# Optimization experiments

Hardware: AMD Instinct MI355X
Metric: run time of the kernel (lower is better)

## Reference

```python
import jax, jax.numpy as jnp
import numpy as np

N_NODES = 30000
IN_DIM = 8
HIDDEN = 64
HEADS1 = 8
OUT_DIM = 8
NEG_SLOPE = 0.2


def _glorot(key, shape):
    fan_in, fan_out = shape[0], shape[-1]
    lim = jnp.sqrt(6.0 / (fan_in + fan_out))
    return jax.random.uniform(key, shape, jnp.float32, -lim, lim)


def setup_inputs() -> dict:
    key = jax.random.key(0)
    ks = jax.random.split(key, 12)
    x = jax.random.normal(ks[0], (N_NODES, IN_DIM), jnp.float32)
    edge_index = jax.random.randint(ks[1], (2, 300000), 0, N_NODES, jnp.int32)
    # layer 1: in=8, out=HIDDEN per head, 8 heads, concat
    W1l = _glorot(ks[2], (IN_DIM, HEADS1 * HIDDEN))
    W1r = _glorot(ks[3], (IN_DIM, HEADS1 * HIDDEN))
    a1 = _glorot(ks[4], (HEADS1, HIDDEN))
    b1 = jnp.zeros((HEADS1 * HIDDEN,), jnp.float32)
    # layer 2: in=HEADS1*HIDDEN, out=OUT_DIM, 1 head
    W2l = _glorot(ks[5], (HEADS1 * HIDDEN, OUT_DIM))
    W2r = _glorot(ks[6], (HEADS1 * HIDDEN, OUT_DIM))
    a2 = _glorot(ks[7], (1, OUT_DIM))
    b2 = jnp.zeros((OUT_DIM,), jnp.float32)
    return {"x": x, "edge_index": edge_index, "W1l": W1l, "W1r": W1r,
            "a1": a1, "b1": b1, "W2l": W2l, "W2r": W2r, "a2": a2, "b2": b2}


def gatv2_layer(x, src, dst, Wl, Wr, att, bias, heads, out_ch):
    n = x.shape[0]
    xl = (x @ Wl).reshape(n, heads, out_ch)   # messages (source side)
    xr = (x @ Wr).reshape(n, heads, out_ch)   # target side
    h = jax.nn.leaky_relu(xl[src] + xr[dst], NEG_SLOPE)   # [E,H,C]
    e = jnp.einsum('ehc,hc->eh', h, att)                  # [E,H]
    # segment softmax over incoming edges per destination node
    m = jax.ops.segment_max(e, dst, num_segments=n)
    p = jnp.exp(e - m[dst])
    denom = jax.ops.segment_sum(p, dst, num_segments=n)
    alpha = p / denom[dst]                                # [E,H]
    out = jax.ops.segment_sum(alpha[..., None] * xl[src], dst, num_segments=n)
    return out.reshape(n, heads * out_ch) + bias


def reference(x, edge_index, W1l, W1r, a1, b1, W2l, W2r, a2, b2):
    n = x.shape[0]
    loops = jnp.arange(n, dtype=edge_index.dtype)
    src = jnp.concatenate([edge_index[0], loops])  # add_self_loops=True (PyG default)
    dst = jnp.concatenate([edge_index[1], loops])
    h = gatv2_layer(x, src, dst, W1l, W1r, a1, b1, HEADS1, HIDDEN)
    h = jax.nn.relu(h)
    out = gatv2_layer(h, src, dst, W2l, W2r, a2, b2, 1, OUT_DIM)
    return out
```

## Files before the change

kernel.cpp:

```cpp
#include <hip/hip_runtime.h>
#include <hip/hip_fp16.h>
#include <math.h>

#define N_NODES   30000
#define N_EDGE    300000
#define N_EDGE_T  330000
#define HEADS     8
#define HIDDEN    64
#define IN_DIM    8
#define OUT_DIM   8
#define NEG_SLOPE 0.2f

#define DPP_ADDF(x, ctrl)                                                     \
    x += __int_as_float(__builtin_amdgcn_update_dpp(                          \
            0, __float_as_int(x), (ctrl), 0xF, 0xF, true))
#define RED16(x) do { DPP_ADDF(x, 0xB1); DPP_ADDF(x, 0x4E);                   \
                      DPP_ADDF(x, 0x141); DPP_ADDF(x, 0x140); } while (0)
#define RED8(x)  do { DPP_ADDF(x, 0xB1); DPP_ADDF(x, 0x4E);                   \
                      DPP_ADDF(x, 0x141); } while (0)


__global__ __launch_bounds__(256) void zero_kernel(int* __restrict__ count) {
    int i = blockIdx.x * 256 + threadIdx.x;
    if (i < N_NODES) count[i] = 0;
}

__global__ __launch_bounds__(256) void count_kernel(const int* __restrict__ ei,
                                                    int* __restrict__ count) {
    int e = blockIdx.x * 256 + threadIdx.x;
    if (e >= N_EDGE_T) return;
    int d = (e < N_EDGE) ? ei[N_EDGE + e] : (e - N_EDGE);
    atomicAdd(&count[d], 1);
}

__global__ __launch_bounds__(1024) void scan_kernel(const int* __restrict__ count,
                                                    int* __restrict__ row_start,
                                                    int* __restrict__ cursor) {
    __shared__ int wsum[16];
    const int tid  = threadIdx.x;
    const int wave = tid >> 6;
    const int lane = tid & 63;
    const int4* c4 = (const int4*)count;
    const int N4 = N_NODES / 4;
    int run = 0;
    for (int r = 0; r < 4; ++r) {
        const int g  = r * 1024 + tid;
        const int i0 = 2 * g;
        const int i1 = 2 * g + 1;
        int4 v0 = make_int4(0,0,0,0), v1 = make_int4(0,0,0,0);
        if (i0 < N4) v0 = c4[i0];
        if (i1 < N4) v1 = c4[i1];
        int s = v0.x + v0.y + v0.z + v0.w + v1.x + v1.y + v1.z + v1.w;
        int sc = s;
        #pragma unroll
        for (int off = 1; off < 64; off <<= 1) {
            int t = __shfl_up(sc, off, 64);
            if (lane >= off) sc += t;
        }
        if (lane == 63) wsum[wave] = sc;
        __syncthreads();
        if (tid < 16) {
            int w = wsum[tid];
            #pragma unroll
            for (int off = 1; off < 16; off <<= 1) {
                int t = __shfl_up(w, off, 64);
                if (tid >= off) w += t;
            }
            wsum[tid] = w;
        }
        __syncthreads();
        const int woff = (wave > 0) ? wsum[wave - 1] : 0;
        int e0 = run + woff + (sc - s);
        int4 ex0, ex1;
        ex0.x = e0;           ex0.y = ex0.x + v0.x;
        ex0.z = ex0.y + v0.y; ex0.w = ex0.z + v0.z;
        int e4 = ex0.w + v0.w;
        ex1.x = e4;           ex1.y = ex1.x + v1.x;
        ex1.z = ex1.y + v1.y; ex1.w = ex1.z + v1.z;
        if (i0 < N4) { ((int4*)row_start)[i0] = ex0; ((int4*)cursor)[i0] = ex0; }
        if (i1 < N4) { ((int4*)row_start)[i1] = ex1; ((int4*)cursor)[i1] = ex1; }
        const int tot = wsum[15];
        __syncthreads();
        run += tot;
    }
    if (tid == 0) row_start[N_NODES] = run;
}

__global__ __launch_bounds__(256) void scatter_kernel(const int* __restrict__ ei,
                                                      int* __restrict__ cursor,
                                                      int* __restrict__ edge_src) {
    int e = blockIdx.x * 256 + threadIdx.x;
    if (e >= N_EDGE_T) return;
    int s, d;
    if (e < N_EDGE) { s = ei[e]; d = ei[N_EDGE + e]; }
    else            { s = d = e - N_EDGE; }
    int pos = atomicAdd(&cursor[d], 1);
    edge_src[pos] = s;
}


__global__ __launch_bounds__(256) void proj_kernel(
    const float* __restrict__ x, const float* __restrict__ W1l,
    __half* __restrict__ xl_h)
{
    const int t    = threadIdx.x;
    const int lane = t & 63;
    float w0[IN_DIM], w1[IN_DIM];
    #pragma unroll
    for (int k = 0; k < IN_DIM; ++k) {
        const float2 wp = *(const float2*)&W1l[k * 512 + 2 * t];
        w0[k] = wp.x; w1[k] = wp.y;
    }
    for (int n = blockIdx.x; n < N_NODES; n += gridDim.x) {
        const float xlane = x[n * IN_DIM + (lane & 7)];
        float l0 = 0.f, l1 = 0.f;
        #pragma unroll
        for (int k = 0; k < IN_DIM; ++k) {
            const float xk = __shfl(xlane, k, 64);
            l0 = fmaf(xk, w0[k], l0);
            l1 = fmaf(xk, w1[k], l1);
        }
        ((__half2*)xl_h)[n * 256 + t] = __floats2half2_rn(l0, l1);
    }
}


__global__ void __launch_bounds__(256, 4)
layer1_kernel(
    const float* __restrict__ x,
    const __half* __restrict__ xl_h, const float* __restrict__ W1r,
    const float* __restrict__ a1,  const float* __restrict__ b1,
    const float* __restrict__ W2l, const float* __restrict__ W2r,
    const int* __restrict__ row_start, const int* __restrict__ edge_src,
    float* __restrict__ xl2, float* __restrict__ xr2)
{
    const int wv   = threadIdx.x >> 6;
    const int lane = threadIdx.x & 63;
    const int d    = blockIdx.x * 4 + wv;
    const int colb = lane * 8;

    const int rse = row_start[d + (lane & 1)];
    const int rs  = __shfl(rse, 0, 64);
    const int re  = __shfl(rse, 1, 64);
    const int deg = re - rs;
    const int nb  = deg < 64 ? deg : 64;

    const int eidx = edge_src[rs + (lane < deg ? lane : deg - 1)];

    const float xlane = x[d * IN_DIM + (lane & 7)];

    float av[8], xr[8];
    { const float4 a0 = *(const float4*)&a1[colb];
      const float4 a4 = *(const float4*)&a1[colb + 4];
      av[0]=a0.x; av[1]=a0.y; av[2]=a0.z; av[3]=a0.w;
      av[4]=a4.x; av[5]=a4.y; av[6]=a4.z; av[7]=a4.w; }
    #pragma unroll
    for (int i = 0; i < 8; ++i) xr[i] = 0.f;
    #pragma unroll
    for (int k = 0; k < IN_DIM; ++k) {
        const float xv = __shfl(xlane, k, 64);
        const float4 r0 = *(const float4*)&W1r[k * 512 + colb];
        const float4 r4 = *(const float4*)&W1r[k * 512 + colb + 4];
        xr[0] = fmaf(xv, r0.x, xr[0]); xr[1] = fmaf(xv, r0.y, xr[1]);
        xr[2] = fmaf(xv, r0.z, xr[2]); xr[3] = fmaf(xv, r0.w, xr[3]);
        xr[4] = fmaf(xv, r4.x, xr[4]); xr[5] = fmaf(xv, r4.y, xr[5]);
        xr[6] = fmaf(xv, r4.z, xr[6]); xr[7] = fmaf(xv, r4.w, xr[7]);
    }

    float denom  = 0.f;
    float acc[8] = {0.f,0.f,0.f,0.f,0.f,0.f,0.f,0.f};

    auto ldraw = [&](int j) -> int4 {
        const int s = __shfl(eidx, j, 64);
        return *(const int4*)(xl_h + (size_t)s * 512 + colb);
    };
    auto edge1 = [&](const int4 r, bool valid) {
        union { int i; __half2 h; } u0, u1, u2, u3;
        u0.i = r.x; u1.i = r.y; u2.i = r.z; u3.i = r.w;
        float rr[8]; float2 f;
        f = __half22float2(u0.h); rr[0] = f.x; rr[1] = f.y;
        f = __half22float2(u1.h); rr[2] = f.x; rr[3] = f.y;
        f = __half22float2(u2.h); rr[4] = f.x; rr[5] = f.y;
        f = __half22float2(u3.h); rr[6] = f.x; rr[7] = f.y;
        float e = 0.f;
        #pragma unroll
        for (int i = 0; i < 8; ++i) {
            const float q = rr[i] + xr[i];
            const float t = fmaxf(q, NEG_SLOPE * q);
            e = fmaf(av[i], t, e);
        }
        RED8(e);
        const float p = valid ? __expf(e) : 0.f;
        denom += p;
        #pragma unroll
        for (int i = 0; i < 8; ++i) acc[i] = fmaf(p, rr[i], acc[i]);
    };

    int4 R0, R1, R2, R3;
    {
        const int m = nb - 1;
        R0 = ldraw(0);
        R1 = ldraw(1 < m ? 1 : m);
        R2 = ldraw(2 < m ? 2 : m);
        R3 = ldraw(3 < m ? 3 : m);
    }
    for (int j = 0;; j += 4) {
        const bool more = j + 4 < nb;
        int4 N0, N1, N2, N3;
        if (more) {
            const int m = nb - 1;
            const int j4 = j + 4;
            N0 = ldraw(j4 < m ? j4 : m);
            N1 = ldraw(j4 + 1 < m ? j4 + 1 : m);
            N2 = ldraw(j4 + 2 < m ? j4 + 2 : m);
            N3 = ldraw(j4 + 3 < m ? j4 + 3 : m);
            __builtin_amdgcn_sched_barrier(0);
        }
        edge1(R0, true);
        edge1(R1, j + 1 < nb);
        edge1(R2, j + 2 < nb);
        edge1(R3, j + 3 < nb);
        if (!more) break;
        R0 = N0; R1 = N1; R2 = N2; R3 = N3;
    }
    for (int j = 64; j < deg; ++j) {
        const int s = edge_src[rs + j];
        const int4 r = *(const int4*)(xl_h + (size_t)s * 512 + colb);
        edge1(r, true);
    }

    const float inv = 1.f / denom;
    float hv[8];
    { const float4 b0 = *(const float4*)&b1[colb];
      const float4 b4 = *(const float4*)&b1[colb + 4];
      hv[0] = fmaxf(fmaf(acc[0], inv, b0.x), 0.f);
      hv[1] = fmaxf(fmaf(acc[1], inv, b0.y), 0.f);
      hv[2] = fmaxf(fmaf(acc[2], inv, b0.z), 0.f);
      hv[3] = fmaxf(fmaf(acc[3], inv, b0.w), 0.f);
      hv[4] = fmaxf(fmaf(acc[4], inv, b4.x), 0.f);
      hv[5] = fmaxf(fmaf(acc[5], inv, b4.y), 0.f);
      hv[6] = fmaxf(fmaf(acc[6], inv, b4.z), 0.f);
      hv[7] = fmaxf(fmaf(acc[7], inv, b4.w), 0.f); }

    float vl[OUT_DIM], vr[OUT_DIM];
    #pragma unroll
    for (int j = 0; j < OUT_DIM; ++j) { vl[j] = 0.f; vr[j] = 0.f; }
    #pragma unroll
    for (int i = 0; i < 8; ++i) {
        const int c = colb + i;
        const float4 l0 = *(const float4*)&W2l[c * OUT_DIM];
        const float4 l1 = *(const float4*)&W2l[c * OUT_DIM + 4];
        const float4 r0 = *(const float4*)&W2r[c * OUT_DIM];
        const float4 r1 = *(const float4*)&W2r[c * OUT_DIM + 4];
        const float h = hv[i];
        vl[0] = fmaf(h, l0.x, vl[0]); vl[1] = fmaf(h, l0.y, vl[1]);
        vl[2] = fmaf(h, l0.z, vl[2]); vl[3] = fmaf(h, l0.w, vl[3]);
        vl[4] = fmaf(h, l1.x, vl[4]); vl[5] = fmaf(h, l1.y, vl[5]);
        vl[6] = fmaf(h, l1.z, vl[6]); vl[7] = fmaf(h, l1.w, vl[7]);
        vr[0] = fmaf(h, r0.x, vr[0]); vr[1] = fmaf(h, r0.y, vr[1]);
        vr[2] = fmaf(h, r0.z, vr[2]); vr[3] = fmaf(h, r0.w, vr[3]);
        vr[4] = fmaf(h, r1.x, vr[4]); vr[5] = fmaf(h, r1.y, vr[5]);
        vr[6] = fmaf(h, r1.z, vr[6]); vr[7] = fmaf(h, r1.w, vr[7]);
    }
    #pragma unroll
    for (int j = 0; j < OUT_DIM; ++j) {
        RED16(vl[j]);
        vl[j] += __shfl_xor(vl[j], 16, 64);
        vl[j] += __shfl_xor(vl[j], 32, 64);
        RED16(vr[j]);
        vr[j] += __shfl_xor(vr[j], 16, 64);
        vr[j] += __shfl_xor(vr[j], 32, 64);
    }
    if (lane == 0) {
        *(float4*)&xl2[d * OUT_DIM]     = make_float4(vl[0], vl[1], vl[2], vl[3]);
        *(float4*)&xl2[d * OUT_DIM + 4] = make_float4(vl[4], vl[5], vl[6], vl[7]);
        *(float4*)&xr2[d * OUT_DIM]     = make_float4(vr[0], vr[1], vr[2], vr[3]);
        *(float4*)&xr2[d * OUT_DIM + 4] = make_float4(vr[4], vr[5], vr[6], vr[7]);
    }
}


__global__ __launch_bounds__(256) void layer2_kernel(
    const float* __restrict__ xl2, const float* __restrict__ xr2,
    const float* __restrict__ a2,  const float* __restrict__ b2,
    const int* __restrict__ row_start, const int* __restrict__ edge_src,
    float* __restrict__ out)
{
    const int wave = threadIdx.x >> 6;
    const int lane = threadIdx.x & 63;
    const int d = blockIdx.x * 4 + wave;
    if (d >= N_NODES) return;
    const int sub = lane >> 3;
    const int c   = lane & 7;

    const int rse = row_start[d + (lane & 1)];
    const int rs  = __shfl(rse, 0, 64);
    const int re  = __shfl(rse, 1, 64);

    const float a_c  = a2[c];
    const float xr_d = xr2[d * OUT_DIM + c];

    int  e0 = rs + sub;      const bool v0 = e0 < re; e0 = v0 ? e0 : re - 1;
    int  e1 = rs + 8 + sub;  const bool v1 = e1 < re; e1 = v1 ? e1 : re - 1;
    const int s0 = edge_src[e0];
    const int s1 = edge_src[e1];
    const float x0 = xl2[s0 * OUT_DIM + c];
    const float x1 = xl2[s1 * OUT_DIM + c];

    const float u0 = x0 + xr_d; const float t0 = fmaxf(u0, NEG_SLOPE * u0);
    const float u1 = x1 + xr_d; const float t1 = fmaxf(u1, NEG_SLOPE * u1);
    float g0 = a_c * t0;
    float g1 = a_c * t1;
    RED8(g0); RED8(g1);
    const float p0 = v0 ? __expf(g0) : 0.f;
    const float p1 = v1 ? __expf(g1) : 0.f;
    float denom = p0 + p1;
    float acc   = fmaf(p1, x1, p0 * x0);

    for (int b = rs + 16; b < re; b += 8) {
        int e = b + sub;
        const bool v = e < re; e = v ? e : re - 1;
        const int s = edge_src[e];
        const float xs = xl2[s * OUT_DIM + c];
        const float u = xs + xr_d;
        const float t = fmaxf(u, NEG_SLOPE * u);
        float g = a_c * t;
        RED8(g);
        const float p = v ? __expf(g) : 0.f;
        denom += p;
        acc = fmaf(p, xs, acc);
    }

    denom += __shfl_xor(denom, 8,  64);  acc += __shfl_xor(acc, 8,  64);
    denom += __shfl_xor(denom, 16, 64);  acc += __shfl_xor(acc, 16, 64);
    denom += __shfl_xor(denom, 32, 64);  acc += __shfl_xor(acc, 32, 64);

    if (sub == 0) out[d * OUT_DIM + c] = acc / denom + b2[c];
}


extern "C" void kernel_launch(void* const* d_in, const int* in_sizes, int n_in,
                              void* d_out, int out_size, void* d_ws, size_t ws_size,
                              hipStream_t stream) {
    const float* x   = (const float*)d_in[0];
    const int*   ei  = (const int*)  d_in[1];
    const float* W1l = (const float*)d_in[2];
    const float* W1r = (const float*)d_in[3];
    const float* a1  = (const float*)d_in[4];
    const float* b1  = (const float*)d_in[5];
    const float* W2l = (const float*)d_in[6];
    const float* W2r = (const float*)d_in[7];
    const float* a2  = (const float*)d_in[8];
    const float* b2  = (const float*)d_in[9];
    float* out = (float*)d_out;

    char* ws = (char*)d_ws;
    size_t off = 0;
    auto carve = [&](size_t bytes) { char* p = ws + off; off += (bytes + 255) & ~size_t(255); return p; };
    int*    count     = (int*)   carve(N_NODES * sizeof(int));
    int*    row_start = (int*)   carve((N_NODES + 1) * sizeof(int));
    int*    cursor    = (int*)   carve(N_NODES * sizeof(int));
    int*    edge_src  = (int*)   carve(N_EDGE_T * sizeof(int));
    float*  xl2       = (float*) carve(N_NODES * OUT_DIM * sizeof(float));
    float*  xr2       = (float*) carve(N_NODES * OUT_DIM * sizeof(float));
    __half* xl_h      = (__half*)carve((size_t)N_NODES * 512 * sizeof(__half));

    proj_kernel   <<<1024, 256, 0, stream>>>(x, W1l, xl_h);
    zero_kernel   <<<(N_NODES  + 255) / 256, 256, 0, stream>>>(count);
    count_kernel  <<<(N_EDGE_T + 255) / 256, 256, 0, stream>>>(ei, count);
    scan_kernel   <<<1, 1024, 0, stream>>>(count, row_start, cursor);
    scatter_kernel<<<(N_EDGE_T + 255) / 256, 256, 0, stream>>>(ei, cursor, edge_src);
    layer1_kernel <<<N_NODES / 4, 256, 0, stream>>>(x, xl_h, W1r, a1, b1, W2l, W2r,
                                                    row_start, edge_src, xl2, xr2);
    layer2_kernel <<<(N_NODES + 3) / 4, 256, 0, stream>>>(xl2, xr2, a2, b2,
                                                          row_start, edge_src, out);
}
```

Baseline: 292.6 us.

## Recompute source projections per edge instead of gathering precomputed fp16 features

Removes the separate projection kernel and its 30000x512 fp16 buffer. Layer 1 now gathers only the 8-float raw input row for each source node and recomputes the W1l projection per edge from register-held weights, broadcasting x values with readlane. The xr term is folded into the projection accumulator and subtracted back out at the end, since the attention weights sum to one. This swaps a heavy per-edge gather of 512 halfs for 64 FMAs per lane per edge and needs many more pinned registers, which may reduce occupancy.

```diff
diff --git a/kernel.cpp b/kernel.cpp
--- a/kernel.cpp
+++ b/kernel.cpp
@@ -1,5 +1,4 @@
 #include <hip/hip_runtime.h>
-#include <hip/hip_fp16.h>
 #include <math.h>
 
 #define N_NODES   30000
@@ -11,6 +10,8 @@
 #define OUT_DIM   8
 #define NEG_SLOPE 0.2f
 
+#define PIN_V(v) asm volatile("" : "+v"(v))
+
 #define DPP_ADDF(x, ctrl)                                                     \
     x += __int_as_float(__builtin_amdgcn_update_dpp(                          \
             0, __float_as_int(x), (ctrl), 0xF, 0xF, true))
@@ -18,6 +19,8 @@
                       DPP_ADDF(x, 0x141); DPP_ADDF(x, 0x140); } while (0)
 #define RED8(x)  do { DPP_ADDF(x, 0xB1); DPP_ADDF(x, 0x4E);                   \
                       DPP_ADDF(x, 0x141); } while (0)
+
+#define BCAST(v, C) __int_as_float(__builtin_amdgcn_readlane(__float_as_int(v), C))
 
 
 __global__ __launch_bounds__(256) void zero_kernel(int* __restrict__ count) {
@@ -99,36 +102,10 @@
 }
 
 
-__global__ __launch_bounds__(256) void proj_kernel(
-    const float* __restrict__ x, const float* __restrict__ W1l,
-    __half* __restrict__ xl_h)
-{
-    const int t    = threadIdx.x;
-    const int lane = t & 63;
-    float w0[IN_DIM], w1[IN_DIM];
-    #pragma unroll
-    for (int k = 0; k < IN_DIM; ++k) {
-        const float2 wp = *(const float2*)&W1l[k * 512 + 2 * t];
-        w0[k] = wp.x; w1[k] = wp.y;
-    }
-    for (int n = blockIdx.x; n < N_NODES; n += gridDim.x) {
-        const float xlane = x[n * IN_DIM + (lane & 7)];
-        float l0 = 0.f, l1 = 0.f;
-        #pragma unroll
-        for (int k = 0; k < IN_DIM; ++k) {
-            const float xk = __shfl(xlane, k, 64);
-            l0 = fmaf(xk, w0[k], l0);
-            l1 = fmaf(xk, w1[k], l1);
-        }
-        ((__half2*)xl_h)[n * 256 + t] = __floats2half2_rn(l0, l1);
-    }
-}
-
-
 __global__ void __launch_bounds__(256, 4)
 layer1_kernel(
     const float* __restrict__ x,
-    const __half* __restrict__ xl_h, const float* __restrict__ W1r,
+    const float* __restrict__ W1l, const float* __restrict__ W1r,
     const float* __restrict__ a1,  const float* __restrict__ b1,
     const float* __restrict__ W2l, const float* __restrict__ W2r,
     const int* __restrict__ row_start, const int* __restrict__ edge_src,
@@ -147,18 +124,28 @@
 
     const int eidx = edge_src[rs + (lane < deg ? lane : deg - 1)];
 
-    const float xlane = x[d * IN_DIM + (lane & 7)];
-
-    float av[8], xr[8];
+    const float xd = x[d * IN_DIM + (lane & 7)];
+
+    float wl[IN_DIM][8];
+    #pragma unroll
+    for (int k = 0; k < IN_DIM; ++k) {
+        const float4 l0 = *(const float4*)&W1l[k * 512 + colb];
+        const float4 l4 = *(const float4*)&W1l[k * 512 + colb + 4];
+        wl[k][0] = l0.x; wl[k][1] = l0.y; wl[k][2] = l0.z; wl[k][3] = l0.w;
+        wl[k][4] = l4.x; wl[k][5] = l4.y; wl[k][6] = l4.z; wl[k][7] = l4.w;
+    }
+    float av[8];
     { const float4 a0 = *(const float4*)&a1[colb];
       const float4 a4 = *(const float4*)&a1[colb + 4];
       av[0]=a0.x; av[1]=a0.y; av[2]=a0.z; av[3]=a0.w;
       av[4]=a4.x; av[5]=a4.y; av[6]=a4.z; av[7]=a4.w; }
+
+    float xr[8];
     #pragma unroll
     for (int i = 0; i < 8; ++i) xr[i] = 0.f;
     #pragma unroll
     for (int k = 0; k < IN_DIM; ++k) {
-        const float xv = __shfl(xlane, k, 64);
+        const float xv = BCAST(xd, k);
         const float4 r0 = *(const float4*)&W1r[k * 512 + colb];
         const float4 r4 = *(const float4*)&W1r[k * 512 + colb + 4];
         xr[0] = fmaf(xv, r0.x, xr[0]); xr[1] = fmaf(xv, r0.y, xr[1]);
@@ -167,80 +154,94 @@
         xr[6] = fmaf(xv, r4.z, xr[6]); xr[7] = fmaf(xv, r4.w, xr[7]);
     }
 
+    #pragma unroll
+    for (int k = 0; k < IN_DIM; ++k) {
+        #pragma unroll
+        for (int i = 0; i < 8; ++i) PIN_V(wl[k][i]);
+    }
+    #pragma unroll
+    for (int i = 0; i < 8; ++i) { PIN_V(av[i]); PIN_V(xr[i]); }
+
     float denom  = 0.f;
     float acc[8] = {0.f,0.f,0.f,0.f,0.f,0.f,0.f,0.f};
 
-    auto ldraw = [&](int j) -> int4 {
-        const int s = __shfl(eidx, j, 64);
-        return *(const int4*)(xl_h + (size_t)s * 512 + colb);
+    auto ldx = [&](int g) -> float {
+        const int sl = __shfl(eidx, (g << 3) + (lane >> 3), 64);
+        return x[(size_t)sl * IN_DIM + (lane & 7)];
     };
-    auto edge1 = [&](const int4 r, bool valid) {
-        union { int i; __half2 h; } u0, u1, u2, u3;
-        u0.i = r.x; u1.i = r.y; u2.i = r.z; u3.i = r.w;
-        float rr[8]; float2 f;
-        f = __half22float2(u0.h); rr[0] = f.x; rr[1] = f.y;
-        f = __half22float2(u1.h); rr[2] = f.x; rr[3] = f.y;
-        f = __half22float2(u2.h); rr[4] = f.x; rr[5] = f.y;
-        f = __half22float2(u3.h); rr[6] = f.x; rr[7] = f.y;
-        float e = 0.f;
-        #pragma unroll
-        for (int i = 0; i < 8; ++i) {
-            const float q = rr[i] + xr[i];
-            const float t = fmaxf(q, NEG_SLOPE * q);
-            e = fmaf(av[i], t, e);
-        }
+
+    auto edge_do = [&](float q0, float q1, float q2, float q3,
+                       float q4, float q5, float q6, float q7, bool valid) {
+        float t, e;
+        t = fmaxf(q0, NEG_SLOPE * q0); e = av[0] * t;
+        t = fmaxf(q1, NEG_SLOPE * q1); e = fmaf(av[1], t, e);
+        t = fmaxf(q2, NEG_SLOPE * q2); e = fmaf(av[2], t, e);
+        t = fmaxf(q3, NEG_SLOPE * q3); e = fmaf(av[3], t, e);
+        t = fmaxf(q4, NEG_SLOPE * q4); e = fmaf(av[4], t, e);
+        t = fmaxf(q5, NEG_SLOPE * q5); e = fmaf(av[5], t, e);
+        t = fmaxf(q6, NEG_SLOPE * q6); e = fmaf(av[6], t, e);
+        t = fmaxf(q7, NEG_SLOPE * q7); e = fmaf(av[7], t, e);
         RED8(e);
         const float p = valid ? __expf(e) : 0.f;
         denom += p;
+        acc[0] = fmaf(p, q0, acc[0]); acc[1] = fmaf(p, q1, acc[1]);
+        acc[2] = fmaf(p, q2, acc[2]); acc[3] = fmaf(p, q3, acc[3]);
+        acc[4] = fmaf(p, q4, acc[4]); acc[5] = fmaf(p, q5, acc[5]);
+        acc[6] = fmaf(p, q6, acc[6]); acc[7] = fmaf(p, q7, acc[7]);
+    };
+
+    float xg = ldx(0);
+    for (int g = 0;; ++g) {
+        const bool more = ((g + 1) << 3) < nb;
+        float xgn;
+        if (more) xgn = ldx(g + 1);
+
         #pragma unroll
-        for (int i = 0; i < 8; ++i) acc[i] = fmaf(p, rr[i], acc[i]);
-    };
-
-    int4 R0, R1, R2, R3;
-    {
-        const int m = nb - 1;
-        R0 = ldraw(0);
-        R1 = ldraw(1 < m ? 1 : m);
-        R2 = ldraw(2 < m ? 2 : m);
-        R3 = ldraw(3 < m ? 3 : m);
-    }
-    for (int j = 0;; j += 4) {
-        const bool more = j + 4 < nb;
-        int4 N0, N1, N2, N3;
-        if (more) {
-            const int m = nb - 1;
-            const int j4 = j + 4;
-            N0 = ldraw(j4 < m ? j4 : m);
-            N1 = ldraw(j4 + 1 < m ? j4 + 1 : m);
-            N2 = ldraw(j4 + 2 < m ? j4 + 2 : m);
-            N3 = ldraw(j4 + 3 < m ? j4 + 3 : m);
-            __builtin_amdgcn_sched_barrier(0);
+        for (int jj = 0; jj < 8; ++jj) {
+            const int j = (g << 3) + jj;
+            float q0 = xr[0], q1 = xr[1], q2 = xr[2], q3 = xr[3];
+            float q4 = xr[4], q5 = xr[5], q6 = xr[6], q7 = xr[7];
+            #pragma unroll
+            for (int k = 0; k < IN_DIM; ++k) {
+                const float xk = BCAST(xg, jj * 8 + k);
+                q0 = fmaf(xk, wl[k][0], q0); q1 = fmaf(xk, wl[k][1], q1);
+                q2 = fmaf(xk, wl[k][2], q2); q3 = fmaf(xk, wl[k][3], q3);
+                q4 = fmaf(xk, wl[k][4], q4); q5 = fmaf(xk, wl[k][5], q5);
+                q6 = fmaf(xk, wl[k][6], q6); q7 = fmaf(xk, wl[k][7], q7);
+            }
+            edge_do(q0, q1, q2, q3, q4, q5, q6, q7, j < nb);
         }
-        edge1(R0, true);
-        edge1(R1, j + 1 < nb);
-        edge1(R2, j + 2 < nb);
-        edge1(R3, j + 3 < nb);
         if (!more) break;
-        R0 = N0; R1 = N1; R2 = N2; R3 = N3;
+        xg = xgn;
     }
     for (int j = 64; j < deg; ++j) {
         const int s = edge_src[rs + j];
-        const int4 r = *(const int4*)(xl_h + (size_t)s * 512 + colb);
-        edge1(r, true);
+        const float xt = x[(size_t)s * IN_DIM + (lane & 7)];
+        float q0 = xr[0], q1 = xr[1], q2 = xr[2], q3 = xr[3];
+        float q4 = xr[4], q5 = xr[5], q6 = xr[6], q7 = xr[7];
+        #pragma unroll
+        for (int k = 0; k < IN_DIM; ++k) {
+            const float xk = BCAST(xt, k);
+            q0 = fmaf(xk, wl[k][0], q0); q1 = fmaf(xk, wl[k][1], q1);
+            q2 = fmaf(xk, wl[k][2], q2); q3 = fmaf(xk, wl[k][3], q3);
+            q4 = fmaf(xk, wl[k][4], q4); q5 = fmaf(xk, wl[k][5], q5);
+            q6 = fmaf(xk, wl[k][6], q6); q7 = fmaf(xk, wl[k][7], q7);
+        }
+        edge_do(q0, q1, q2, q3, q4, q5, q6, q7, true);
     }
 
     const float inv = 1.f / denom;
     float hv[8];
     { const float4 b0 = *(const float4*)&b1[colb];
       const float4 b4 = *(const float4*)&b1[colb + 4];
-      hv[0] = fmaxf(fmaf(acc[0], inv, b0.x), 0.f);
-      hv[1] = fmaxf(fmaf(acc[1], inv, b0.y), 0.f);
-      hv[2] = fmaxf(fmaf(acc[2], inv, b0.z), 0.f);
-      hv[3] = fmaxf(fmaf(acc[3], inv, b0.w), 0.f);
-      hv[4] = fmaxf(fmaf(acc[4], inv, b4.x), 0.f);
-      hv[5] = fmaxf(fmaf(acc[5], inv, b4.y), 0.f);
-      hv[6] = fmaxf(fmaf(acc[6], inv, b4.z), 0.f);
-      hv[7] = fmaxf(fmaf(acc[7], inv, b4.w), 0.f); }
+      hv[0] = fmaxf(fmaf(acc[0], inv, b0.x - xr[0]), 0.f);
+      hv[1] = fmaxf(fmaf(acc[1], inv, b0.y - xr[1]), 0.f);
+      hv[2] = fmaxf(fmaf(acc[2], inv, b0.z - xr[2]), 0.f);
+      hv[3] = fmaxf(fmaf(acc[3], inv, b0.w - xr[3]), 0.f);
+      hv[4] = fmaxf(fmaf(acc[4], inv, b4.x - xr[4]), 0.f);
+      hv[5] = fmaxf(fmaf(acc[5], inv, b4.y - xr[5]), 0.f);
+      hv[6] = fmaxf(fmaf(acc[6], inv, b4.z - xr[6]), 0.f);
+      hv[7] = fmaxf(fmaf(acc[7], inv, b4.w - xr[7]), 0.f); }
 
     float vl[OUT_DIM], vr[OUT_DIM];
     #pragma unroll
@@ -357,20 +358,18 @@
     char* ws = (char*)d_ws;
     size_t off = 0;
     auto carve = [&](size_t bytes) { char* p = ws + off; off += (bytes + 255) & ~size_t(255); return p; };
-    int*    count     = (int*)   carve(N_NODES * sizeof(int));
-    int*    row_start = (int*)   carve((N_NODES + 1) * sizeof(int));
-    int*    cursor    = (int*)   carve(N_NODES * sizeof(int));
-    int*    edge_src  = (int*)   carve(N_EDGE_T * sizeof(int));
-    float*  xl2       = (float*) carve(N_NODES * OUT_DIM * sizeof(float));
-    float*  xr2       = (float*) carve(N_NODES * OUT_DIM * sizeof(float));
-    __half* xl_h      = (__half*)carve((size_t)N_NODES * 512 * sizeof(__half));
-
-    proj_kernel   <<<1024, 256, 0, stream>>>(x, W1l, xl_h);
+    int*   count     = (int*)  carve(N_NODES * sizeof(int));
+    int*   row_start = (int*)  carve((N_NODES + 1) * sizeof(int));
+    int*   cursor    = (int*)  carve(N_NODES * sizeof(int));
+    int*   edge_src  = (int*)  carve(N_EDGE_T * sizeof(int));
+    float* xl2       = (float*)carve(N_NODES * OUT_DIM * sizeof(float));
+    float* xr2       = (float*)carve(N_NODES * OUT_DIM * sizeof(float));
+
     zero_kernel   <<<(N_NODES  + 255) / 256, 256, 0, stream>>>(count);
     count_kernel  <<<(N_EDGE_T + 255) / 256, 256, 0, stream>>>(ei, count);
     scan_kernel   <<<1, 1024, 0, stream>>>(count, row_start, cursor);
     scatter_kernel<<<(N_EDGE_T + 255) / 256, 256, 0, stream>>>(ei, cursor, edge_src);
-    layer1_kernel <<<N_NODES / 4, 256, 0, stream>>>(x, xl_h, W1r, a1, b1, W2l, W2r,
+    layer1_kernel <<<N_NODES / 4, 256, 0, stream>>>(x, W1l, W1r, a1, b1, W2l, W2r,
                                                     row_start, edge_src, xl2, xr2);
     layer2_kernel <<<(N_NODES + 3) / 4, 256, 0, stream>>>(xl2, xr2, a2, b2,
                                                           row_start, edge_src, out);
```

After: 266.2 us. 1.1x faster.
